# Optimization experiments

Hardware: AMD Instinct MI355X
Metric: run time of the kernel (lower is better)

## Reference

```python
import jax, jax.numpy as jnp
import numpy as np
from jax import lax

B, T = 16384, 10
CAR, REG, POI, WEEK, TIME = 500000, 10000, 64, 7, 1440
H, LBL = 256, 512


def setup_inputs() -> dict:
    key = jax.random.key(0)
    ks = jax.random.split(key, 32)
    p = lambda i, shp: jax.random.normal(ks[i], shp, jnp.float32) * 0.05
    d = {}
    d["region_idx"] = jax.random.randint(ks[0], (B, T), 0, REG)
    d["poi_idx"] = jax.random.randint(ks[1], (B, T), 0, POI)
    d["car_idx"] = jax.random.randint(ks[2], (B,), 0, CAR)
    d["week_idx"] = jax.random.randint(ks[3], (B,), 0, WEEK)
    d["time_idx"] = jax.random.randint(ks[4], (B,), 0, TIME)
    d["coords"] = jax.random.normal(ks[5], (B, T, 2), jnp.float32)
    d["region_tbl"] = p(6, (REG, 8))
    d["poi_tbl"] = p(7, (POI, 4))
    d["car_tbl"] = p(8, (CAR, 16))
    d["week_tbl"] = p(9, (WEEK, 3))
    d["time_tbl"] = p(10, (TIME, 8))
    d["W_rp"] = p(11, (12, 32)); d["b_rp"] = p(12, (32,))
    d["W_co"] = p(13, (2, 8));  d["b_co"] = p(14, (8,))
    d["conv_w"] = p(15, (3, 40, 32)); d["conv_b"] = p(16, (32,))
    # 2-layer LSTM (torch gate order i,f,g,o), input 59, hidden 256
    d["Wih0"] = p(17, (4 * H, 59)); d["Whh0"] = p(18, (4 * H, H))
    d["bih0"] = p(19, (4 * H,));    d["bhh0"] = p(20, (4 * H,))
    d["Wih1"] = p(21, (4 * H, H)); d["Whh1"] = p(22, (4 * H, H))
    d["bih1"] = p(23, (4 * H,));   d["bhh1"] = p(24, (4 * H,))
    d["W1"] = p(25, (H, 512));    d["b1"] = p(26, (512,))
    d["W2"] = p(27, (512, 1024)); d["b2"] = p(28, (1024,))
    d["W3"] = p(29, (1024, LBL)); d["b3"] = p(30, (LBL,))
    return d


def _lstm_layer(x, Wih, Whh, bih, bhh):
    Bx, Hh = x.shape[0], Whh.shape[1]
    bias = bih + bhh

    def step(carry, xt):
        h, c = carry
        g = xt @ Wih.T + h @ Whh.T + bias
        i, f, gg, o = jnp.split(g, 4, axis=-1)
        c = jax.nn.sigmoid(f) * c + jax.nn.sigmoid(i) * jnp.tanh(gg)
        h = jax.nn.sigmoid(o) * jnp.tanh(c)
        return (h, c), h

    h0 = jnp.zeros((Bx, Hh), x.dtype)
    _, hs = lax.scan(step, (h0, h0), jnp.swapaxes(x, 0, 1))
    return jnp.swapaxes(hs, 0, 1)


def reference(region_idx, poi_idx, car_idx, week_idx, time_idx, coords,
              region_tbl, poi_tbl, car_tbl, week_tbl, time_tbl,
              W_rp, b_rp, W_co, b_co, conv_w, conv_b,
              Wih0, Whh0, bih0, bhh0, Wih1, Whh1, bih1, bhh1,
              W1, b1, W2, b2, W3, b3):
    # batched embedding gathers (replaces per-item python-loop lookups)
    rp = jnp.concatenate([region_tbl[region_idx], poi_tbl[poi_idx]], -1)   # [B,T,12]
    nv = jnp.concatenate([rp @ W_rp + b_rp, coords @ W_co + b_co], -1)     # [B,T,40]
    conv = jax.nn.elu(
        lax.conv_general_dilated(nv, conv_w, (1,), 'VALID',
                                 dimension_numbers=('NWC', 'WIO', 'NWC')) + conv_b)  # [B,T-2,32]
    emb = jnp.tanh(jnp.concatenate(
        [car_tbl[car_idx], week_tbl[week_idx], time_tbl[time_idx]], -1))   # [B,27]
    x = jnp.concatenate(
        [conv, jnp.broadcast_to(emb[:, None, :], conv.shape[:2] + (27,))], -1)  # [B,T-2,59]
    h = _lstm_layer(x, Wih0, Whh0, bih0, bhh0)
    h = _lstm_layer(h, Wih1, Whh1, bih1, bhh1)
    last = h[:, -1, :]                                                     # [B,256]
    # nn.Sequential of three Linears with NO activations between
    return ((last @ W1 + b1) @ W2 + b2) @ W3 + b3                          # [B,LBL]
```

## Files before the change

### kernel.cpp

```cpp
#include <hip/hip_runtime.h>
#include <hip/hip_bf16.h>
#include <math.h>

#define B_SZ 16384
#define T_CONV 8
#define HID 256
#define SK 16

typedef __bf16 bf16x8 __attribute__((ext_vector_type(8)));
typedef float f32x4 __attribute__((ext_vector_type(4)));

__device__ __forceinline__ float fsigm(float x) { return 1.f / (1.f + __expf(-x)); }
__device__ __forceinline__ float ftanh(float x) {
    float t = __expf(-2.f * fabsf(x));
    float r = (1.f - t) / (1.f + t);
    return x >= 0.f ? r : -r;
}

__global__ void collapse_conv(const float* __restrict__ W_rp, const float* __restrict__ b_rp,
                              const float* __restrict__ W_co, const float* __restrict__ b_co,
                              const float* __restrict__ conv_w, const float* __restrict__ conv_b,
                              float* __restrict__ Crp, float* __restrict__ Cco,
                              float* __restrict__ cb2)
{
    int idx = blockIdx.x * 256 + threadIdx.x;
    if (idx < 1152) {
        int o = idx & 31, k = (idx >> 5) % 12, dt = idx / 384;
        float a = 0.f;
        for (int c = 0; c < 32; c++) a += W_rp[k * 32 + c] * conv_w[(dt * 40 + c) * 32 + o];
        Crp[idx] = a;
    } else if (idx < 1344) {
        int j = idx - 1152;
        int o = j & 31, k = (j >> 5) & 1, dt = j / 64;
        float a = 0.f;
        for (int c = 0; c < 8; c++) a += W_co[k * 8 + c] * conv_w[(dt * 40 + 32 + c) * 32 + o];
        Cco[j] = a;
    } else if (idx < 1376) {
        int o = idx - 1344;
        float a = conv_b[o];
        for (int dt = 0; dt < 3; dt++) {
            for (int c = 0; c < 32; c++) a += b_rp[c] * conv_w[(dt * 40 + c) * 32 + o];
            for (int c = 0; c < 8; c++)  a += b_co[c] * conv_w[(dt * 40 + 32 + c) * 32 + o];
        }
        cb2[o] = a;
    }
}

#define FB_SAMPLES 4
__global__ __launch_bounds__(256) void feature_kernel(
    const int* __restrict__ region_idx, const int* __restrict__ poi_idx,
    const int* __restrict__ car_idx, const int* __restrict__ week_idx,
    const int* __restrict__ time_idx, const float* __restrict__ coords,
    const float* __restrict__ region_tbl, const float* __restrict__ poi_tbl,
    const float* __restrict__ car_tbl, const float* __restrict__ week_tbl,
    const float* __restrict__ time_tbl,
    const float* __restrict__ Crp, const float* __restrict__ Cco,
    const float* __restrict__ cb2, __bf16* __restrict__ Xp)
{
    __shared__ float s_crp[1152];
    __shared__ float s_cco[192];
    __shared__ float s_cb2[32];
    __shared__ float s_rp[FB_SAMPLES][10][12];
    __shared__ float s_co[FB_SAMPLES][10][2];
    __shared__ float s_emb[FB_SAMPLES][27];

    int tid = threadIdx.x;
    for (int i = tid; i < 1152; i += 256) s_crp[i] = Crp[i];
    if (tid < 192) s_cco[tid] = Cco[tid];
    else if (tid < 224) s_cb2[tid - 192] = cb2[tid - 192];

    int s  = tid >> 6;
    int lt = tid & 63;
    int b  = blockIdx.x * FB_SAMPLES + s;

    if (lt < 27) {
        float v;
        if (lt < 16)      v = car_tbl[(size_t)car_idx[b] * 16 + lt];
        else if (lt < 19) v = week_tbl[week_idx[b] * 3 + (lt - 16)];
        else              v = time_tbl[time_idx[b] * 8 + (lt - 19)];
        s_emb[s][lt] = tanhf(v);
    }
    for (int i = lt; i < 120; i += 64) {
        int t = i / 12, k = i % 12;
        float v;
        if (k < 8) v = region_tbl[(size_t)region_idx[b * 10 + t] * 8 + k];
        else       v = poi_tbl[poi_idx[b * 10 + t] * 4 + (k - 8)];
        s_rp[s][t][k] = v;
    }
    for (int i = lt; i < 20; i += 64) {
        int t = i >> 1, k = i & 1;
        s_co[s][t][k] = coords[(size_t)(b * 10 + t) * 2 + k];
    }
    __syncthreads();

    for (int i = lt; i < 256; i += 64) {
        int t = i >> 5, o = i & 31;
        float acc = s_cb2[o];
        #pragma unroll
        for (int dt = 0; dt < 3; dt++) {
            #pragma unroll
            for (int k = 0; k < 12; k++)
                acc += s_rp[s][t + dt][k] * s_crp[(dt * 12 + k) * 32 + o];
            acc += s_co[s][t + dt][0] * s_cco[(dt * 2 + 0) * 32 + o]
                 + s_co[s][t + dt][1] * s_cco[(dt * 2 + 1) * 32 + o];
        }
        acc = acc > 0.f ? acc : expm1f(acc);
        Xp[(size_t)(b * 8 + t) * 64 + o] = (__bf16)acc;
    }
    for (int i = lt; i < 216; i += 64) {
        int t = i / 27, j = i % 27;
        Xp[(size_t)(b * 8 + t) * 64 + 32 + j] = (__bf16)s_emb[s][j];
    }
    for (int i = lt; i < 40; i += 64) {
        int t = i / 5, j = i % 5;
        Xp[(size_t)(b * 8 + t) * 64 + 59 + j] = (__bf16)0.f;
    }
}

#define AST 40
__global__ __launch_bounds__(256, 2) void lstm_fused(
    const __bf16* __restrict__ A1, int lda1, int K1,
    const __bf16* __restrict__ A2, int lda2,
    const __bf16* __restrict__ WS,
    const float* __restrict__ bias, float* __restrict__ cst,
    __bf16* __restrict__ hb,
    int KT, int is_t0)
{
    __shared__ __align__(16) unsigned char smem[4 * 16 * 68 * 4];
    __bf16* As = (__bf16*)smem;
    float*  GL = (float*)smem;

    int tid = threadIdx.x;
    int bm  = blockIdx.y * 64;
    int bnf = blockIdx.x * 4;
    int bn  = blockIdx.x * 64;
    int l   = tid & 63;
    int g   = tid >> 6;
    int fr  = l & 15;
    int fo  = (l >> 4) * 8;

    f32x4 acc[4][4] = {};

    int s_row = tid >> 2;
    int s_q   = tid & 3;

    auto asrc = [&](int kt) -> const __bf16* {
        int k0 = kt * 32;
        if (k0 < K1) return A1 + (size_t)(bm + s_row) * lda1 + k0 + s_q * 8;
        return A2 + (size_t)(bm + s_row) * lda2 + (k0 - K1) + s_q * 8;
    };
    const __bf16* wbase = WS + ((size_t)g * 16 + bnf) * 512 + (size_t)l * 8;

    { *(bf16x8*)&As[s_row * AST + s_q * 8] = *(const bf16x8*)asrc(0); }
    bf16x8 bcur[4];
    #pragma unroll
    for (int j = 0; j < 4; j++) bcur[j] = *(const bf16x8*)(wbase + j * 512);

    for (int kt = 0; kt < KT; kt++) {
        int cb = kt & 1;
        bf16x8 bnxt[4], an0;
        if (kt + 1 < KT) {
            an0 = *(const bf16x8*)asrc(kt + 1);
            const __bf16* wb = wbase + (size_t)(kt + 1) * 32768;
            #pragma unroll
            for (int j = 0; j < 4; j++) bnxt[j] = *(const bf16x8*)(wb + j * 512);
        }
        __syncthreads();
        bf16x8 af[4];
        #pragma unroll
        for (int mf = 0; mf < 4; mf++)
            af[mf] = *(bf16x8*)&As[cb * 64 * AST + (mf * 16 + fr) * AST + fo];
        #pragma unroll
        for (int mf = 0; mf < 4; mf++)
            #pragma unroll
            for (int j = 0; j < 4; j++)
                acc[mf][j] = __builtin_amdgcn_mfma_f32_16x16x32_bf16(
                    af[mf], bcur[j], acc[mf][j], 0, 0, 0);
        if (kt + 1 < KT) {
            *(bf16x8*)&As[(cb ^ 1) * 64 * AST + s_row * AST + s_q * 8] = an0;
            #pragma unroll
            for (int j = 0; j < 4; j++) bcur[j] = bnxt[j];
        }
    }

    int rbase = (l >> 4) * 4;
    int prow  = tid >> 4;
    int pcol  = (tid & 15) * 4;
    f32x4 bs[4];
    #pragma unroll
    for (int gg = 0; gg < 4; gg++)
        bs[gg] = *(const f32x4*)&bias[gg * 256 + bn + pcol];

    #pragma unroll
    for (int mf = 0; mf < 4; mf++) {
        __syncthreads();
        #pragma unroll
        for (int j = 0; j < 4; j++)
            #pragma unroll
            for (int e = 0; e < 4; e++)
                GL[(g * 16 + rbase + e) * 68 + j * 16 + fr] = acc[mf][j][e];
        __syncthreads();

        size_t moff = ((size_t)bm + mf * 16 + prow) * 256 + bn + pcol;
        f32x4 gi = *(f32x4*)&GL[(0 * 16 + prow) * 68 + pcol];
        f32x4 gf = *(f32x4*)&GL[(1 * 16 + prow) * 68 + pcol];
        f32x4 gg = *(f32x4*)&GL[(2 * 16 + prow) * 68 + pcol];
        f32x4 go = *(f32x4*)&GL[(3 * 16 + prow) * 68 + pcol];
        f32x4 cold = {0.f, 0.f, 0.f, 0.f};
        if (!is_t0) cold = *(f32x4*)&cst[moff];
        f32x4 cn;
        union { unsigned short u[4]; unsigned long long v; } hx;
        #pragma unroll
        for (int q = 0; q < 4; q++) {
            float i_ = fsigm(gi[q] + bs[0][q]);
            float f_ = fsigm(gf[q] + bs[1][q]);
            float g_ = ftanh(gg[q] + bs[2][q]);
            float o_ = fsigm(go[q] + bs[3][q]);
            float c_ = f_ * cold[q] + i_ * g_;
            cn[q] = c_;
            float h_ = o_ * ftanh(c_);
            __bf16 hv = (__bf16)h_;
            hx.u[q] = *(unsigned short*)&hv;
        }
        *(f32x4*)&cst[moff] = cn;
        *(unsigned long long*)&hb[moff] = hx.v;
    }
}

#define HAST 40
__global__ __launch_bounds__(256, 2) void head_mfma(
    const __bf16* __restrict__ A,
    const __bf16* __restrict__ WS,
    const float* __restrict__ bias, float* __restrict__ out)
{
    __shared__ __align__(16) __bf16 As[2][128 * HAST];

    int tid = threadIdx.x;
    int bm  = blockIdx.y * 128;
    int l   = tid & 63;
    int wv  = tid >> 6;
    int fr  = l & 15;
    int fo  = (l >> 4) * 8;
    int nfb = blockIdx.x * 16 + wv * 4;

    f32x4 acc[8][4] = {};

    int s_row  = tid >> 1;
    int s_half = tid & 1;
    const __bf16* abase = A + (size_t)(bm + s_row) * 256 + s_half * 16;
    const __bf16* wbase = WS + (size_t)nfb * 512 + (size_t)l * 8;

    {
        bf16x8 v0 = *(const bf16x8*)abase;
        bf16x8 v1 = *(const bf16x8*)(abase + 8);
        *(bf16x8*)&As[0][s_row * HAST + s_half * 16]     = v0;
        *(bf16x8*)&As[0][s_row * HAST + s_half * 16 + 8] = v1;
    }
    bf16x8 bcur[4];
    #pragma unroll
    for (int j = 0; j < 4; j++) bcur[j] = *(const bf16x8*)(wbase + j * 512);

    #pragma unroll
    for (int kt = 0; kt < 8; kt++) {
        int cb = kt & 1;
        bf16x8 bnxt[4], an0, an1;
        if (kt + 1 < 8) {
            const __bf16* s = abase + (kt + 1) * 32;
            an0 = *(const bf16x8*)s;
            an1 = *(const bf16x8*)(s + 8);
            const __bf16* wb = wbase + (size_t)(kt + 1) * 16384;
            #pragma unroll
            for (int j = 0; j < 4; j++) bnxt[j] = *(const bf16x8*)(wb + j * 512);
        }
        __syncthreads();
        bf16x8 af[8];
        #pragma unroll
        for (int mf = 0; mf < 8; mf++)
            af[mf] = *(bf16x8*)&As[cb][(mf * 16 + fr) * HAST + fo];
        #pragma unroll
        for (int mf = 0; mf < 8; mf++)
            #pragma unroll
            for (int j = 0; j < 4; j++)
                acc[mf][j] = __builtin_amdgcn_mfma_f32_16x16x32_bf16(
                    af[mf], bcur[j], acc[mf][j], 0, 0, 0);
        if (kt + 1 < 8) {
            *(bf16x8*)&As[cb ^ 1][s_row * HAST + s_half * 16]     = an0;
            *(bf16x8*)&As[cb ^ 1][s_row * HAST + s_half * 16 + 8] = an1;
            #pragma unroll
            for (int j = 0; j < 4; j++) bcur[j] = bnxt[j];
        }
    }

    int rbase = (l >> 4) * 4;
    #pragma unroll
    for (int mf = 0; mf < 8; mf++) {
        #pragma unroll
        for (int j = 0; j < 4; j++) {
            int n = (nfb + j) * 16 + fr;
            float bv = bias[n];
            #pragma unroll
            for (int e = 0; e < 4; e++) {
                size_t m = (size_t)bm + mf * 16 + rbase + e;
                out[m * 512 + n] = acc[mf][j][e] + bv;
            }
        }
    }
}

__global__ __launch_bounds__(256) void gemm_nn_sk(
    const float* __restrict__ A, int lda, const float* __restrict__ Bm, int ldb,
    float* __restrict__ P, int M, int N, int K)
{
    __shared__ float As[16][68];
    __shared__ float Bs[16][68];
    int tid = threadIdx.x;
    int tx = tid & 15, ty = tid >> 4;
    int bm = blockIdx.y * 64, bn = blockIdx.x * 64;
    int klen = K / SK;
    int kbeg = blockIdx.z * klen;

    float acc[4][4] = {};

    for (int k0 = kbeg; k0 < kbeg + klen; k0 += 16) {
        for (int i = tid; i < 1024; i += 256) {
            int k = i & 15, m = i >> 4;
            As[k][m] = A[(size_t)(bm + m) * lda + k0 + k];
        }
        for (int i = tid; i < 1024; i += 256) {
            int n = i & 63, k = i >> 6;
            Bs[k][n] = Bm[(size_t)(k0 + k) * ldb + bn + n];
        }
        __syncthreads();
        #pragma unroll
        for (int kk = 0; kk < 16; kk++) {
            float4 a = *(const float4*)&As[kk][ty * 4];
            float4 b = *(const float4*)&Bs[kk][tx * 4];
            float av[4] = {a.x, a.y, a.z, a.w};
            float bv[4] = {b.x, b.y, b.z, b.w};
            #pragma unroll
            for (int i = 0; i < 4; i++)
                #pragma unroll
                for (int j = 0; j < 4; j++)
                    acc[i][j] += av[i] * bv[j];
        }
        __syncthreads();
    }

    float* Pd = P + (size_t)blockIdx.z * M * N;
    #pragma unroll
    for (int i = 0; i < 4; i++) {
        int m = bm + ty * 4 + i;
        #pragma unroll
        for (int j = 0; j < 4; j++) {
            int n = bn + tx * 4 + j;
            Pd[(size_t)m * N + n] = acc[i][j];
        }
    }
}

__global__ __launch_bounds__(256) void reduce_sk(
    const float* __restrict__ P, int MN, float* __restrict__ C)
{
    int i = blockIdx.x * 256 + threadIdx.x;
    if (i >= MN) return;
    float a = 0.f;
    #pragma unroll
    for (int s = 0; s < SK; s++) a += P[(size_t)s * MN + i];
    C[i] = a;
}

__global__ __launch_bounds__(256) void vecmat(
    const float* __restrict__ v, const float* __restrict__ M, int ldb, int K,
    const float* __restrict__ bias, float* __restrict__ outv)
{
    __shared__ float red[4][64];
    int l = threadIdx.x & 63;
    int w = threadIdx.x >> 6;
    int n = blockIdx.x * 64 + l;
    int kpw = K >> 2;
    int k0 = w * kpw;

    float p[8] = {};
    for (int k = k0; k < k0 + kpw; k += 8) {
        #pragma unroll
        for (int u = 0; u < 8; u++)
            p[u] += v[k + u] * M[(size_t)(k + u) * ldb + n];
    }
    red[w][l] = ((p[0] + p[1]) + (p[2] + p[3])) + ((p[4] + p[5]) + (p[6] + p[7]));
    __syncthreads();
    if (w == 0)
        outv[n] = red[0][l] + red[1][l] + red[2][l] + red[3][l]
                + (bias ? bias[n] : 0.f);
}

__global__ void add_biases(const float* __restrict__ bih0, const float* __restrict__ bhh0,
                           const float* __restrict__ bih1, const float* __restrict__ bhh1,
                           float* __restrict__ b01)
{
    int i = blockIdx.x * 256 + threadIdx.x;
    if (i < 1024)       b01[i] = bih0[i] + bhh0[i];
    else if (i < 2048)  b01[i] = bih1[i - 1024] + bhh1[i - 1024];
}

__global__ void pack_w01_swz(const float* __restrict__ Wih0, const float* __restrict__ Whh0,
                             const float* __restrict__ Wih1, const float* __restrict__ Whh1,
                             __bf16* __restrict__ WS0, __bf16* __restrict__ WS1)
{
    const int N0 = 10 * 4 * 16 * 64 * 8;
    const int N1 = 16 * 4 * 16 * 64 * 8;
    int idx = blockIdx.x * 256 + threadIdx.x;
    if (idx < N0) {
        int e  = idx & 7;
        int l  = (idx >> 3) & 63;
        int nf = (idx >> 9) & 15;
        int g  = (idx >> 13) & 3;
        int kt = idx >> 15;
        int n_row = g * 256 + nf * 16 + (l & 15);
        int k = kt * 32 + ((l >> 4) * 8) + e;
        float v = (k < 59) ? Wih0[(size_t)n_row * 59 + k]
                : (k < 64) ? 0.f
                           : Whh0[(size_t)n_row * 256 + (k - 64)];
        WS0[idx] = (__bf16)v;
    } else if (idx < N0 + N1) {
        int j = idx - N0;
        int e  = j & 7;
        int l  = (j >> 3) & 63;
        int nf = (j >> 9) & 15;
        int g  = (j >> 13) & 3;
        int kt = j >> 15;
        int n_row = g * 256 + nf * 16 + (l & 15);
        int k = kt * 32 + ((l >> 4) * 8) + e;
        float v = (k < 256) ? Wih1[(size_t)n_row * 256 + k]
                            : Whh1[(size_t)n_row * 256 + (k - 256)];
        WS1[j] = (__bf16)v;
    }
}

__global__ void pack_head_swz(const float* __restrict__ Wc, __bf16* __restrict__ WS)
{
    int idx = blockIdx.x * 256 + threadIdx.x;
    if (idx >= 8 * 32 * 64 * 8) return;
    int e  = idx & 7;
    int l  = (idx >> 3) & 63;
    int nf = (idx >> 9) & 31;
    int kt = idx >> 14;
    int n = nf * 16 + (l & 15);
    int k = kt * 32 + ((l >> 4) * 8) + e;
    WS[idx] = (__bf16)Wc[(size_t)k * 512 + n];
}

extern "C" void kernel_launch(void* const* d_in, const int* in_sizes, int n_in,
                              void* d_out, int out_size, void* d_ws, size_t ws_size,
                              hipStream_t stream)
{
    const int*   region_idx = (const int*)d_in[0];
    const int*   poi_idx    = (const int*)d_in[1];
    const int*   car_idx    = (const int*)d_in[2];
    const int*   week_idx   = (const int*)d_in[3];
    const int*   time_idx   = (const int*)d_in[4];
    const float* coords     = (const float*)d_in[5];
    const float* region_tbl = (const float*)d_in[6];
    const float* poi_tbl    = (const float*)d_in[7];
    const float* car_tbl    = (const float*)d_in[8];
    const float* week_tbl   = (const float*)d_in[9];
    const float* time_tbl   = (const float*)d_in[10];
    const float* W_rp   = (const float*)d_in[11];
    const float* b_rp   = (const float*)d_in[12];
    const float* W_co   = (const float*)d_in[13];
    const float* b_co   = (const float*)d_in[14];
    const float* conv_w = (const float*)d_in[15];
    const float* conv_b = (const float*)d_in[16];
    const float* Wih0 = (const float*)d_in[17];
    const float* Whh0 = (const float*)d_in[18];
    const float* bih0 = (const float*)d_in[19];
    const float* bhh0 = (const float*)d_in[20];
    const float* Wih1 = (const float*)d_in[21];
    const float* Whh1 = (const float*)d_in[22];
    const float* bih1 = (const float*)d_in[23];
    const float* bhh1 = (const float*)d_in[24];
    const float* W1 = (const float*)d_in[25];
    const float* b1 = (const float*)d_in[26];
    const float* W2 = (const float*)d_in[27];
    const float* b2 = (const float*)d_in[28];
    const float* W3 = (const float*)d_in[29];
    const float* b3 = (const float*)d_in[30];
    float* out = (float*)d_out;

    char* ws = (char*)d_ws;
    size_t off = 0;
    auto alloc = [&](size_t bytes) -> char* {
        char* p = ws + off;
        off = (off + bytes + 255) & ~(size_t)255;
        return p;
    };
    __bf16* Xp   = (__bf16*)alloc((size_t)B_SZ * 8 * 64 * 2);
    __bf16* h0b  = (__bf16*)alloc((size_t)B_SZ * HID * 2);
    __bf16* h1b  = (__bf16*)alloc((size_t)B_SZ * HID * 2);
    float*  c0   = (float*)alloc((size_t)B_SZ * HID * 4);
    float*  c1   = (float*)alloc((size_t)B_SZ * HID * 4);
    __bf16* WS0  = (__bf16*)alloc((size_t)10 * 4 * 16 * 64 * 8 * 2);
    __bf16* WS1  = (__bf16*)alloc((size_t)16 * 4 * 16 * 64 * 8 * 2);
    __bf16* WSH  = (__bf16*)alloc((size_t)8 * 32 * 64 * 8 * 2);
    float*  T1    = (float*)alloc(256 * 1024 * 4);
    float*  tb1   = (float*)alloc(1024 * 4);
    float*  Wcomb = (float*)alloc(256 * 512 * 4);
    float*  bcomb = (float*)alloc(512 * 4);
    float*  b01   = (float*)alloc(2048 * 4);
    float*  Crp   = (float*)alloc(1152 * 4);
    float*  Cco   = (float*)alloc(192 * 4);
    float*  cb2   = (float*)alloc(32 * 4);
    float*  Psk   = (float*)alloc((size_t)SK * 256 * 1024 * 4);
    (void)ws_size;
    float* bias0 = b01;
    float* bias1 = b01 + 1024;

    pack_w01_swz<<<3328, 256, 0, stream>>>(Wih0, Whh0, Wih1, Whh1, WS0, WS1);
    add_biases<<<8, 256, 0, stream>>>(bih0, bhh0, bih1, bhh1, b01);
    collapse_conv<<<6, 256, 0, stream>>>(W_rp, b_rp, W_co, b_co, conv_w, conv_b,
                                         Crp, Cco, cb2);

    gemm_nn_sk<<<dim3(16, 4, SK), 256, 0, stream>>>(W1, 512, W2, 1024, Psk, 256, 1024, 512);
    reduce_sk<<<(256 * 1024 + 255) / 256, 256, 0, stream>>>(Psk, 256 * 1024, T1);
    vecmat<<<16, 256, 0, stream>>>(b1, W2, 1024, 512, b2, tb1);
    gemm_nn_sk<<<dim3(8, 4, SK), 256, 0, stream>>>(T1, 1024, W3, 512, Psk, 256, 512, 1024);
    reduce_sk<<<(256 * 512 + 255) / 256, 256, 0, stream>>>(Psk, 256 * 512, Wcomb);
    vecmat<<<8, 256, 0, stream>>>(tb1, W3, 512, 1024, b3, bcomb);
    pack_head_swz<<<512, 256, 0, stream>>>(Wcomb, WSH);

    feature_kernel<<<B_SZ / FB_SAMPLES, 256, 0, stream>>>(
        region_idx, poi_idx, car_idx, week_idx, time_idx, coords,
        region_tbl, poi_tbl, car_tbl, week_tbl, time_tbl,
        Crp, Cco, cb2, Xp);

    dim3 lstm_grid(4, B_SZ / 64);
    for (int t = 0; t < T_CONV; t++) {
        lstm_fused<<<lstm_grid, 256, 0, stream>>>(
            Xp + (size_t)t * 64, 8 * 64, 64,
            h0b, HID,
            WS0, bias0, c0, h0b,
            t == 0 ? 2 : 10, t == 0);

        lstm_fused<<<lstm_grid, 256, 0, stream>>>(
            h0b, HID, 256,
            h1b, HID,
            WS1, bias1, c1, h1b,
            t == 0 ? 8 : 16, t == 0);
    }

    head_mfma<<<dim3(2, 128), 256, 0, stream>>>(h1b, WSH, bcomb, out);
}
```

Measured before the change: 534.2 us.

## Wavefront-schedule LSTM layers so layer1 step t runs with layer0 step t+1

Merges layer 1 at step t and layer 0 at step t+1 into one launch using a z-dimension split, with ping-pong hidden-state buffers so the two do not conflict. This cuts the number of serial LSTM launches from 16 to 9 and doubles the blocks per launch, which helps fill the GPU and reduces launch and tail overhead. It costs extra hidden-state buffers and relies on correct buffer parity indexing.

```diff
diff --git a/kernel.cpp b/kernel.cpp
--- a/kernel.cpp
+++ b/kernel.cpp
@@ -118,7 +118,8 @@
 }
 
 #define AST 40
-__global__ __launch_bounds__(256, 2) void lstm_fused(
+__device__ __forceinline__ void lstm_body(
+    unsigned char* smem,
     const __bf16* __restrict__ A1, int lda1, int K1,
     const __bf16* __restrict__ A2, int lda2,
     const __bf16* __restrict__ WS,
@@ -126,7 +127,6 @@
     __bf16* __restrict__ hb,
     int KT, int is_t0)
 {
-    __shared__ __align__(16) unsigned char smem[4 * 16 * 68 * 4];
     __bf16* As = (__bf16*)smem;
     float*  GL = (float*)smem;
 
@@ -225,6 +225,30 @@
         *(f32x4*)&cst[moff] = cn;
         *(unsigned long long*)&hb[moff] = hx.v;
     }
+}
+
+__global__ __launch_bounds__(256, 2) void lstm_fused(
+    const __bf16* __restrict__ A1, int lda1, int K1,
+    const __bf16* __restrict__ A2, int lda2,
+    const __bf16* __restrict__ WS,
+    const float* __restrict__ bias, float* __restrict__ cst,
+    __bf16* __restrict__ hb, int KT, int is_t0)
+{
+    __shared__ __align__(16) unsigned char smem[4 * 16 * 68 * 4];
+    lstm_body(smem, A1, lda1, K1, A2, lda2, WS, bias, cst, hb, KT, is_t0);
+}
+
+__global__ __launch_bounds__(256, 2) void lstm_dual(
+    const __bf16* A1a, int lda1a, int K1a, const __bf16* A2a, int lda2a,
+    const __bf16* WSa, const float* biasa, float* csta, __bf16* hba, int KTa, int t0a,
+    const __bf16* A1b, int lda1b, int K1b, const __bf16* A2b, int lda2b,
+    const __bf16* WSb, const float* biasb, float* cstb, __bf16* hbb, int KTb, int t0b)
+{
+    __shared__ __align__(16) unsigned char smem[4 * 16 * 68 * 4];
+    if (blockIdx.z == 0)
+        lstm_body(smem, A1a, lda1a, K1a, A2a, lda2a, WSa, biasa, csta, hba, KTa, t0a);
+    else
+        lstm_body(smem, A1b, lda1b, K1b, A2b, lda2b, WSb, biasb, cstb, hbb, KTb, t0b);
 }
 
 #define HAST 40
@@ -494,8 +518,10 @@
         return p;
     };
     __bf16* Xp   = (__bf16*)alloc((size_t)B_SZ * 8 * 64 * 2);
-    __bf16* h0b  = (__bf16*)alloc((size_t)B_SZ * HID * 2);
-    __bf16* h1b  = (__bf16*)alloc((size_t)B_SZ * HID * 2);
+    __bf16* H0a  = (__bf16*)alloc((size_t)B_SZ * HID * 2);
+    __bf16* H0b  = (__bf16*)alloc((size_t)B_SZ * HID * 2);
+    __bf16* H1a  = (__bf16*)alloc((size_t)B_SZ * HID * 2);
+    __bf16* H1b  = (__bf16*)alloc((size_t)B_SZ * HID * 2);
     float*  c0   = (float*)alloc((size_t)B_SZ * HID * 4);
     float*  c1   = (float*)alloc((size_t)B_SZ * HID * 4);
     __bf16* WS0  = (__bf16*)alloc((size_t)10 * 4 * 16 * 64 * 8 * 2);
@@ -513,6 +539,8 @@
     (void)ws_size;
     float* bias0 = b01;
     float* bias1 = b01 + 1024;
+    __bf16* H0[2] = {H0a, H0b};
+    __bf16* H1[2] = {H1a, H1b};
 
     pack_w01_swz<<<3328, 256, 0, stream>>>(Wih0, Whh0, Wih1, Whh1, WS0, WS1);
     add_biases<<<8, 256, 0, stream>>>(bih0, bhh0, bih1, bhh1, b01);
@@ -533,19 +561,22 @@
         Crp, Cco, cb2, Xp);
 
     dim3 lstm_grid(4, B_SZ / 64);
-    for (int t = 0; t < T_CONV; t++) {
-        lstm_fused<<<lstm_grid, 256, 0, stream>>>(
-            Xp + (size_t)t * 64, 8 * 64, 64,
-            h0b, HID,
-            WS0, bias0, c0, h0b,
-            t == 0 ? 2 : 10, t == 0);
-
-        lstm_fused<<<lstm_grid, 256, 0, stream>>>(
-            h0b, HID, 256,
-            h1b, HID,
-            WS1, bias1, c1, h1b,
-            t == 0 ? 8 : 16, t == 0);
-    }
-
-    head_mfma<<<dim3(2, 128), 256, 0, stream>>>(h1b, WSH, bcomb, out);
-}
+    dim3 dual_grid(4, B_SZ / 64, 2);
+
+    lstm_fused<<<lstm_grid, 256, 0, stream>>>(
+        Xp, 512, 64, H0[1], HID, WS0, bias0, c0, H0[0], 2, 1);
+
+    for (int t = 0; t < T_CONV - 1; t++) {
+        int pc = t & 1, pn = (t + 1) & 1;
+        lstm_dual<<<dual_grid, 256, 0, stream>>>(
+            H0[pc], HID, 256, H1[pn], HID, WS1, bias1, c1, H1[pc],
+            (t == 0) ? 8 : 16, t == 0,
+            Xp + (size_t)(t + 1) * 64, 512, 64, H0[pc], HID, WS0, bias0, c0, H0[pn],
+            10, 0);
+    }
+
+    lstm_fused<<<lstm_grid, 256, 0, stream>>>(
+        H0[1], HID, 256, H1[0], HID, WS1, bias1, c1, H1[1], 16, 0);
+
+    head_mfma<<<dim3(2, 128), 256, 0, stream>>>(H1[1], WSH, bcomb, out);
+}
```

Result: faster. 502.5 us, median of 3 (-5.9%).
